# Kernel tuning notes

Hardware: AMD Instinct MI355X
Metric: run time of the kernel (lower is better)

## Reference

```python
import jax, jax.numpy as jnp
import numpy as np

EPS = 1e-5

def _layernorm(x, g, b):
    m = jnp.mean(x, axis=-1, keepdims=True)
    v = jnp.mean((x - m) ** 2, axis=-1, keepdims=True)
    return (x - m) * jax.lax.rsqrt(v + EPS) * g + b

def setup_inputs() -> dict:
    key = jax.random.key(0)
    ks = jax.random.split(key, 6)
    B, N, D, H, F = 4, 4096, 256, 256, 1024
    s = lambda d: 1.0 / np.sqrt(d)
    return {
        "x": jax.random.normal(ks[0], (B, N, D), jnp.float32),
        "ln1_g": jnp.ones((D,), jnp.float32),
        "ln1_b": jnp.zeros((D,), jnp.float32),
        "wq": jax.random.normal(ks[1], (D, H), jnp.float32) * s(D),
        "bq": jnp.zeros((H,), jnp.float32),
        "wk": jax.random.normal(ks[2], (D, H), jnp.float32) * s(D),
        "bk": jnp.zeros((H,), jnp.float32),
        "wv": jax.random.normal(ks[3], (D, D), jnp.float32) * s(D),
        "bv": jnp.zeros((D,), jnp.float32),
        "ln2_g": jnp.ones((D,), jnp.float32),
        "ln2_b": jnp.zeros((D,), jnp.float32),
        "w1": jax.random.normal(ks[4], (D, F), jnp.float32) * s(D),
        "b1": jnp.zeros((F,), jnp.float32),
        "w2": jax.random.normal(ks[5], (F, D), jnp.float32) * s(F),
        "b2": jnp.zeros((D,), jnp.float32),
    }

def reference(x, ln1_g, ln1_b, wq, bq, wk, bk, wv, bv, ln2_g, ln2_b, w1, b1, w2, b2):
    hdim = wq.shape[1]
    x = _layernorm(x, ln1_g, ln1_b)                      # [B,N,D]
    q = x @ wq + bq                                      # [B,N,H]
    k = x @ wk + bk                                      # [B,N,H]
    v = x @ wv + bv                                      # [B,N,D]
    att = jnp.einsum('bnh,bmh->bnm', q, k) / jnp.sqrt(jnp.float32(hdim))
    att = jax.nn.softmax(att, axis=-1)                   # [B,N,N]
    x = jnp.einsum('bnm,bmd->bnd', att, v) + x           # residual around attention
    h = _layernorm(x, ln2_g, ln2_b)
    h = jax.nn.relu(h @ w1 + b1) @ w2 + b2
    return h + x
```

## Files before the change

### kernel.cpp

```cpp
#include <hip/hip_runtime.h>
#include <stdint.h>

typedef unsigned short u16;
typedef __attribute__((ext_vector_type(8))) short short8;
typedef __attribute__((ext_vector_type(4))) float f32x4;
typedef __attribute__((ext_vector_type(16))) float f32x16;

__device__ __forceinline__ u16 f2b(float f){
  union { float f; unsigned u; } x; x.f = f;
  unsigned r = x.u + 0x7FFFu + ((x.u >> 16) & 1u);
  return (u16)(r >> 16);
}
__device__ __forceinline__ float b2f(u16 u){
  return __uint_as_float(((unsigned)u) << 16);
}

__device__ __forceinline__ unsigned cvtpk_bf16(float lo, float hi){
  unsigned r;
  asm("v_cvt_pk_bf16_f32 %0, %1, %2" : "=v"(r) : "v"(lo), "v"(hi));
  return r;
}

__device__ __forceinline__ void gload_lds16(const void* g, void* l){
  __builtin_amdgcn_global_load_lds(
      (const __attribute__((address_space(1))) unsigned int*)g,
      (__attribute__((address_space(3))) unsigned int*)l, 16, 0, 0);
}

__global__ void __launch_bounds__(256) transpose_all(const float* __restrict__ wq,
                                                     const float* __restrict__ wk,
                                                     const float* __restrict__ wv,
                                                     const float* __restrict__ w1,
                                                     const float* __restrict__ w2,
                                                     u16* __restrict__ wqkvT,
                                                     u16* __restrict__ w1T,
                                                     u16* __restrict__ w2T){
  __shared__ float sm[32][33];
  int id = blockIdx.x;
  const float* in; u16* out; int K, N, kx, ny;
  if (id < 192){
    int j = id >> 6, r = id & 63;
    in = (j==0) ? wq : (j==1) ? wk : wv;
    out = wqkvT + (size_t)j*65536; K = 256; N = 256; kx = r>>3; ny = r&7;
  } else if (id < 448){
    int r = id - 192; in = w1; out = w1T; K = 256; N = 1024; kx = r&7; ny = r>>3;
  } else {
    int r = id - 448; in = w2; out = w2T; K = 1024; N = 256; kx = r>>3; ny = r&7;
  }
  int k0 = kx*32, n0 = ny*32;
  int t = threadIdx.x; int tr = t>>5, tc = t&31;
  #pragma unroll
  for (int p=0;p<4;p++) sm[p*8+tr][tc] = in[(size_t)(k0+p*8+tr)*N + n0+tc];
  __syncthreads();
  #pragma unroll
  for (int p=0;p<4;p++) out[(size_t)(n0+p*8+tr)*K + k0+tc] = f2b(sm[tc][p*8+tr]);
}

__global__ void __launch_bounds__(256) ln_kernel(const float* __restrict__ in,
                                                 const float* __restrict__ g,
                                                 const float* __restrict__ bb,
                                                 float* __restrict__ outF,
                                                 u16* __restrict__ outB){
  int row = blockIdx.x, t = threadIdx.x;
  size_t base = (size_t)row*256;
  float v = in[base + t];
  float s = v;
  #pragma unroll
  for (int m=1;m<64;m<<=1) s += __shfl_xor(s, m);
  __shared__ float red[4];
  int w = t>>6;
  if ((t&63)==0) red[w] = s;
  __syncthreads();
  float mean = (red[0]+red[1]+red[2]+red[3]) * (1.0f/256.0f);
  float d = v - mean;
  float s2 = d*d;
  #pragma unroll
  for (int m=1;m<64;m<<=1) s2 += __shfl_xor(s2, m);
  __syncthreads();
  if ((t&63)==0) red[w] = s2;
  __syncthreads();
  float var = (red[0]+red[1]+red[2]+red[3]) * (1.0f/256.0f);
  float y = d * rsqrtf(var + 1e-5f) * g[t] + bb[t];
  if (outF) outF[base+t] = y;
  outB[base+t] = f2b(y);
}

template<int MODE>
__global__ void __launch_bounds__(256, 2) gemm_bt(const u16* __restrict__ A,
                                                  const u16* __restrict__ BT,
                                                  const float* __restrict__ bias,
                                                  const float* __restrict__ bias2,
                                                  const float* __restrict__ bias3,
                                                  const u16* __restrict__ res,
                                                  float* __restrict__ outF,
                                                  u16* __restrict__ outB,
                                                  u16* __restrict__ outB2,
                                                  u16* __restrict__ outB3,
                                                  int M, int N, int K){
  __shared__ u16 As[128*64];
  __shared__ u16 Bs[128*64];
  int tid = threadIdx.x;
  int m0 = blockIdx.x*128, n0 = blockIdx.y*128;
  int wave = tid>>6, lane = tid&63, lr = lane&15, lg = lane>>4;
  int wm = (wave>>1)*64, wn = (wave&1)*64;

  f32x4 acc[4][4];
  #pragma unroll
  for (int i=0;i<4;i++)
    #pragma unroll
    for (int j=0;j<4;j++) acc[i][j] = (f32x4){0.f,0.f,0.f,0.f};

  int nk = K >> 6;
  for (int kt=0; kt<nk; ++kt){
    __syncthreads();
    #pragma unroll
    for (int i=0;i<4;i++){
      int de = i*256 + tid; int row = de>>3; int ch = de&7; int sc = ch ^ (row&7);
      gload_lds16(A + (size_t)(m0+row)*K + kt*64 + sc*8, (char*)As + de*16);
    }
    #pragma unroll
    for (int i=0;i<4;i++){
      int de = i*256 + tid; int row = de>>3; int ch = de&7; int sc = ch ^ (row&7);
      gload_lds16(BT + (size_t)(n0+row)*K + kt*64 + sc*8, (char*)Bs + de*16);
    }
    asm volatile("s_waitcnt vmcnt(0)" ::: "memory");
    __syncthreads();
    #pragma unroll
    for (int kk=0;kk<2;kk++){
      short8 af[4], bf[4];
      #pragma unroll
      for (int mi=0;mi<4;mi++){
        int row = wm + mi*16 + lr;
        int c = (kk*4 + lg) ^ (row&7);
        af[mi] = *(const short8*)&As[row*64 + c*8];
      }
      #pragma unroll
      for (int ni=0;ni<4;ni++){
        int row = wn + ni*16 + lr;
        int c = (kk*4 + lg) ^ (row&7);
        bf[ni] = *(const short8*)&Bs[row*64 + c*8];
      }
      #pragma unroll
      for (int mi=0;mi<4;mi++)
        #pragma unroll
        for (int ni=0;ni<4;ni++)
          acc[mi][ni] = __builtin_amdgcn_mfma_f32_16x16x32_bf16(af[mi], bf[ni], acc[mi][ni], 0,0,0);
    }
  }
  #pragma unroll
  for (int mi=0;mi<4;mi++)
    #pragma unroll
    for (int ni=0;ni<4;ni++)
      #pragma unroll
      for (int r=0;r<4;r++){
        int row = m0 + wm + mi*16 + lg*4 + r;
        int col = n0 + wn + ni*16 + lr;
        if (MODE==3){
          int seg = n0 >> 8;
          int c2 = col & 255;
          float bb = (seg==0) ? bias[c2] : (seg==1) ? bias2[c2] : bias3[c2];
          float vout = acc[mi][ni][r] + bb;
          if (seg==0)      outB [(size_t)row*256 + c2] = f2b(vout);
          else if (seg==1) outB2[(size_t)row*256 + c2] = f2b(vout);
          else {
            size_t gaddr = ((size_t)(row>>12)<<20)
                         + ((((size_t)((row&4095)>>3)<<8) + (size_t)c2)<<3) + (row&7);
            outB3[gaddr] = f2b(vout);
          }
        } else {
          float vout = acc[mi][ni][r] + bias[col];
          if (MODE==1) vout = fmaxf(vout, 0.f);
          if (MODE==2) outF[(size_t)row*N + col] = vout + b2f(res[(size_t)row*N + col]);
          else         outB[(size_t)row*N + col] = f2b(vout);
        }
      }
}

__device__ __forceinline__ void stage_tiles(const u16* __restrict__ Kb,
                                            const u16* __restrict__ Vt,
                                            int b, int kv0,
                                            char* Kdst, char* Vdst, int tid){
  #pragma unroll
  for (int i=0;i<4;i++){
    int de = i*256 + tid; int kv = de>>5; int c = de&31; int sc = c ^ (kv&7);
    gload_lds16(Kb + (((size_t)(b*4096 + kv0 + kv))<<8) + sc*8, Kdst + (size_t)de*16);
  }
  #pragma unroll
  for (int i=0;i<4;i++){
    int de = i*256 + tid; int kvc = de>>8; int d = de&255;
    gload_lds16(Vt + ((((size_t)b*512 + (kv0>>3) + kvc)<<8) + (size_t)d)*8,
                Vdst + (size_t)de*16);
  }
}

__global__ void __launch_bounds__(256, 2) flash_attn32(const u16* __restrict__ Qb,
                                                       const u16* __restrict__ Kb,
                                                       const u16* __restrict__ Vt,
                                                       u16* __restrict__ Opart,
                                                       float* __restrict__ MLpart){
  __shared__ __align__(16) char smem[74752];
  const int NC = 4096;
  int tid = threadIdx.x, wave = tid>>6, lane = tid&63;
  int lq = lane & 31, hi = lane >> 5;
  int b = blockIdx.y, s = blockIdx.z;
  int qb0 = blockIdx.x*128 + wave*32;
  int kvbeg = s*1024;
  const int NT = 32;
  u16* PsW = (u16*)(smem + 65536) + wave*32*36;

  short8 qf[16];
  {
    const u16* qbase = Qb + (((size_t)b*NC + qb0 + lq)<<8) + hi*8;
    #pragma unroll
    for (int ks=0; ks<16; ks++) qf[ks] = *(const short8*)(qbase + ks*16);
  }

  f32x16 o[8];
  #pragma unroll
  for (int i=0;i<8;i++)
    o[i] = (f32x16){0.f,0.f,0.f,0.f,0.f,0.f,0.f,0.f,0.f,0.f,0.f,0.f,0.f,0.f,0.f,0.f};
  float mrun = -__builtin_inff(), ell = 0.f;

  stage_tiles(Kb, Vt, b, kvbeg, smem, smem + 16384, tid);
  asm volatile("s_waitcnt vmcnt(0)" ::: "memory");
  __syncthreads();

  for (int t=0; t<NT; t++){
    char* Kc = smem + ((t&1) ? 32768 : 0);
    char* Vc = Kc + 16384;
    char* Kn = smem + ((t&1) ? 0 : 32768);
    char* Vn = Kn + 16384;
    int kv0 = kvbeg + t*32;
    if (t+1 < NT) stage_tiles(Kb, Vt, b, kv0+32, Kn, Vn, tid);

    f32x16 sacc = (f32x16){0.f,0.f,0.f,0.f,0.f,0.f,0.f,0.f,0.f,0.f,0.f,0.f,0.f,0.f,0.f,0.f};
    __builtin_amdgcn_s_setprio(1);
    #pragma unroll
    for (int ks=0; ks<16; ks++){
      int c = ks*2 + hi;
      short8 kf = *(const short8*)(Kc + lq*512 + ((c ^ (lq&7))<<4));
      sacc = __builtin_amdgcn_mfma_f32_32x32x16_bf16(kf, qf[ks], sacc, 0,0,0);
    }
    __builtin_amdgcn_s_setprio(0);

    float tmax = sacc[0];
    #pragma unroll
    for (int r=1;r<16;r++) tmax = fmaxf(tmax, sacc[r]);
    tmax *= 0.0625f;
    tmax = fmaxf(tmax, __shfl_xor(tmax, 32));
    if (!__all(tmax <= mrun + 8.f)){
      float mn = fmaxf(mrun, tmax);
      float sc = __expf(mrun - mn);
      mrun = mn; ell *= sc;
      #pragma unroll
      for (int r=0;r<16;r++){
        float scr = __shfl(sc, (r&3)+8*(r>>2)+4*hi);
        #pragma unroll
        for (int dt=0; dt<8; dt++) o[dt][r] *= scr;
      }
    }

    float rs = 0.f;
    #pragma unroll
    for (int h=0; h<2; h++){
      float p[8];
      #pragma unroll
      for (int r=0;r<8;r++){ p[r] = __expf(sacc[h*8+r]*0.0625f - mrun); rs += p[r]; }
      uint2 w0, w1;
      w0.x = cvtpk_bf16(p[0], p[1]);  w0.y = cvtpk_bf16(p[2], p[3]);
      w1.x = cvtpk_bf16(p[4], p[5]);  w1.y = cvtpk_bf16(p[6], p[7]);
      *(uint2*)(PsW + lq*36 + h*16 + hi*4)     = w0;
      *(uint2*)(PsW + lq*36 + h*16 + 8 + hi*4) = w1;
    }
    rs += __shfl_xor(rs, 32);
    ell += rs;
    asm volatile("s_waitcnt lgkmcnt(0)" ::: "memory");
    __builtin_amdgcn_sched_barrier(0);
    union { uint2 u2[2]; short8 s8; } pc0, pc1;
    pc0.u2[0] = *(const uint2*)(PsW + lq*36 + hi*8);
    pc0.u2[1] = *(const uint2*)(PsW + lq*36 + hi*8 + 4);
    pc1.u2[0] = *(const uint2*)(PsW + lq*36 + 16 + hi*8);
    pc1.u2[1] = *(const uint2*)(PsW + lq*36 + 16 + hi*8 + 4);
    short8 pa0 = pc0.s8, pa1 = pc1.s8;

    __builtin_amdgcn_s_setprio(1);
    #pragma unroll
    for (int dt=0; dt<8; dt++){
      short8 vf0 = *(const short8*)(Vc + (((hi  )*256 + dt*32 + lq)<<4));
      short8 vf1 = *(const short8*)(Vc + (((2+hi)*256 + dt*32 + lq)<<4));
      o[dt] = __builtin_amdgcn_mfma_f32_32x32x16_bf16(pa0, vf0, o[dt], 0,0,0);
      o[dt] = __builtin_amdgcn_mfma_f32_32x32x16_bf16(pa1, vf1, o[dt], 0,0,0);
    }
    __builtin_amdgcn_s_setprio(0);

    asm volatile("s_waitcnt vmcnt(0)" ::: "memory");
    __syncthreads();
  }

  size_t rowb = (size_t)s*16384 + (size_t)b*NC + qb0;
  #pragma unroll
  for (int dt=0; dt<8; dt++)
    #pragma unroll
    for (int r=0;r<16;r++){
      int q = (r&3) + 8*(r>>2) + 4*hi;
      Opart[(rowb + q)*256 + dt*32 + lq] = f2b(o[dt][r]);
    }
  if (lane < 32){
    MLpart[(rowb + lane)*2]     = mrun;
    MLpart[(rowb + lane)*2 + 1] = ell;
  }
}

__global__ void __launch_bounds__(256) merge4_ln(const u16* __restrict__ Opart,
                                                 const float* __restrict__ MLpart,
                                                 const float* __restrict__ xln,
                                                 const float* __restrict__ g2,
                                                 const float* __restrict__ be2,
                                                 u16* __restrict__ x2b,
                                                 u16* __restrict__ h2){
  int row = blockIdx.x; int t = threadIdx.x;
  const size_t RS = 16384ull*256;
  float m[4], l[4];
  #pragma unroll
  for (int s=0;s<4;s++){
    m[s] = MLpart[((size_t)s*16384 + row)*2];
    l[s] = MLpart[((size_t)s*16384 + row)*2 + 1];
  }
  float M = fmaxf(fmaxf(m[0],m[1]), fmaxf(m[2],m[3]));
  float e[4]; float den = 0.f;
  #pragma unroll
  for (int s=0;s<4;s++){ e[s] = __expf(m[s]-M); den += l[s]*e[s]; }
  float inv = 1.0f/den;
  size_t idx = (size_t)row*256 + t;
  float v = 0.f;
  #pragma unroll
  for (int s=0;s<4;s++) v += b2f(Opart[(size_t)s*RS + idx]) * e[s];
  v = v*inv + xln[idx];
  x2b[idx] = f2b(v);
  float s1 = v;
  #pragma unroll
  for (int mk=1;mk<64;mk<<=1) s1 += __shfl_xor(s1, mk);
  __shared__ float red[4];
  int w = t>>6;
  if ((t&63)==0) red[w] = s1;
  __syncthreads();
  float mean = (red[0]+red[1]+red[2]+red[3]) * (1.0f/256.0f);
  float d = v - mean;
  float s2 = d*d;
  #pragma unroll
  for (int mk=1;mk<64;mk<<=1) s2 += __shfl_xor(s2, mk);
  __syncthreads();
  if ((t&63)==0) red[w] = s2;
  __syncthreads();
  float var = (red[0]+red[1]+red[2]+red[3]) * (1.0f/256.0f);
  h2[idx] = f2b(d * rsqrtf(var + 1e-5f) * g2[t] + be2[t]);
}

extern "C" void kernel_launch(void* const* d_in, const int* in_sizes, int n_in,
                              void* d_out, int out_size, void* d_ws, size_t ws_size,
                              hipStream_t stream){
  const float* x   = (const float*)d_in[0];
  const float* g1  = (const float*)d_in[1];
  const float* be1 = (const float*)d_in[2];
  const float* wq  = (const float*)d_in[3];
  const float* bq  = (const float*)d_in[4];
  const float* wk  = (const float*)d_in[5];
  const float* bk  = (const float*)d_in[6];
  const float* wv  = (const float*)d_in[7];
  const float* bv  = (const float*)d_in[8];
  const float* g2  = (const float*)d_in[9];
  const float* be2 = (const float*)d_in[10];
  const float* w1  = (const float*)d_in[11];
  const float* bm1 = (const float*)d_in[12];
  const float* w2  = (const float*)d_in[13];
  const float* bm2 = (const float*)d_in[14];
  float* out = (float*)d_out;

  const size_t RS = 16384ull*256;
  char* p = (char*)d_ws;
  float* xln = (float*)p;  p += RS*4;
  u16*  Op   = (u16*)p;    p += 4*RS*2;
  float* ML  = (float*)p;  p += 4*16384ull*2*4;
  u16* xb  = (u16*)p; p += RS*2;
  u16* qb  = (u16*)p; p += RS*2;
  u16* kb  = (u16*)p; p += RS*2;
  u16* vT  = (u16*)p; p += RS*2;
  u16* x2b = (u16*)p; p += RS*2;
  u16* wqkvT = (u16*)p; p += 3*65536ull*2;
  u16* w1T = (u16*)p; p += 262144ull*2;
  u16* w2T = (u16*)p; p += 262144ull*2;
  u16*   h1 = Op;
  u16*   h2 = qb;

  transpose_all<<<704, 256, 0, stream>>>(wq, wk, wv, w1, w2, wqkvT, w1T, w2T);

  ln_kernel<<<16384,256,0,stream>>>(x, g1, be1, xln, xb);

  gemm_bt<3><<<dim3(128,6),256,0,stream>>>(xb, wqkvT, bq, bk, bv, nullptr, nullptr,
                                           qb, kb, vT, 16384,768,256);

  flash_attn32<<<dim3(32,4,4),256,0,stream>>>(qb, kb, vT, Op, ML);
  merge4_ln<<<16384,256,0,stream>>>(Op, ML, xln, g2, be2, x2b, h2);

  gemm_bt<1><<<dim3(128,8),256,0,stream>>>(h2, w1T, bm1, nullptr, nullptr, nullptr, nullptr,
                                           h1, nullptr, nullptr, 16384,1024,256);
  gemm_bt<2><<<dim3(128,2),256,0,stream>>>(h1, w2T, bm2, nullptr, nullptr, x2b, out,
                                           nullptr, nullptr, nullptr, 16384,256,1024);
}
```

Before: 167.1 us.

## Keep softmax P in registers by permuting the V layout to match accumulators

Removes the per-wave LDS round trip that converted the S accumulator layout into the MFMA A-operand layout for P. Instead, the P values are packed straight from registers, and the projection kernel writes the transposed V with a permuted row order so the kv index matches the accumulator ordering. This drops the LDS writes, the lgkmcnt wait and the LDS reads in each tile, and shrinks shared memory, which may help occupancy. The risk is correctness: the permutation has to agree exactly with the MFMA output register mapping.

```diff
diff --git a/kernel.cpp b/kernel.cpp
--- a/kernel.cpp
+++ b/kernel.cpp
@@ -163,8 +163,12 @@
           if (seg==0)      outB [(size_t)row*256 + c2] = f2b(vout);
           else if (seg==1) outB2[(size_t)row*256 + c2] = f2b(vout);
           else {
-            size_t gaddr = ((size_t)(row>>12)<<20)
-                         + ((((size_t)((row&4095)>>3)<<8) + (size_t)c2)<<3) + (row&7);
+            int n = row & 4095;
+            int u = n & 31;
+            int g = ((u>>2)&1) | (((u>>4)&1)<<1);
+            int j = (u&3) | (((u>>3)&1)<<2);
+            size_t gran = (size_t)((n>>5)<<2) + g;
+            size_t gaddr = ((size_t)(row>>12)<<20) + (((gran<<8) + (size_t)c2)<<3) + j;
             outB3[gaddr] = f2b(vout);
           }
         } else {
@@ -198,7 +202,7 @@
                                                        const u16* __restrict__ Vt,
                                                        u16* __restrict__ Opart,
                                                        float* __restrict__ MLpart){
-  __shared__ __align__(16) char smem[74752];
+  __shared__ __align__(16) char smem[65536];
   const int NC = 4096;
   int tid = threadIdx.x, wave = tid>>6, lane = tid&63;
   int lq = lane & 31, hi = lane >> 5;
@@ -206,7 +210,6 @@
   int qb0 = blockIdx.x*128 + wave*32;
   int kvbeg = s*1024;
   const int NT = 32;
-  u16* PsW = (u16*)(smem + 65536) + wave*32*36;
 
   short8 qf[16];
   {
@@ -261,27 +264,18 @@
     }
 
     float rs = 0.f;
-    #pragma unroll
-    for (int h=0; h<2; h++){
-      float p[8];
-      #pragma unroll
-      for (int r=0;r<8;r++){ p[r] = __expf(sacc[h*8+r]*0.0625f - mrun); rs += p[r]; }
-      uint2 w0, w1;
-      w0.x = cvtpk_bf16(p[0], p[1]);  w0.y = cvtpk_bf16(p[2], p[3]);
-      w1.x = cvtpk_bf16(p[4], p[5]);  w1.y = cvtpk_bf16(p[6], p[7]);
-      *(uint2*)(PsW + lq*36 + h*16 + hi*4)     = w0;
-      *(uint2*)(PsW + lq*36 + h*16 + 8 + hi*4) = w1;
-    }
+    float pv[16];
+    #pragma unroll
+    for (int r=0;r<16;r++){ pv[r] = __expf(sacc[r]*0.0625f - mrun); rs += pv[r]; }
     rs += __shfl_xor(rs, 32);
     ell += rs;
-    asm volatile("s_waitcnt lgkmcnt(0)" ::: "memory");
-    __builtin_amdgcn_sched_barrier(0);
-    union { uint2 u2[2]; short8 s8; } pc0, pc1;
-    pc0.u2[0] = *(const uint2*)(PsW + lq*36 + hi*8);
-    pc0.u2[1] = *(const uint2*)(PsW + lq*36 + hi*8 + 4);
-    pc1.u2[0] = *(const uint2*)(PsW + lq*36 + 16 + hi*8);
-    pc1.u2[1] = *(const uint2*)(PsW + lq*36 + 16 + hi*8 + 4);
-    short8 pa0 = pc0.s8, pa1 = pc1.s8;
+    union { unsigned w[4]; short8 s; } c0, c1;
+    #pragma unroll
+    for (int r=0;r<4;r++){
+      c0.w[r] = cvtpk_bf16(pv[2*r],   pv[2*r+1]);
+      c1.w[r] = cvtpk_bf16(pv[8+2*r], pv[8+2*r+1]);
+    }
+    short8 pa0 = c0.s, pa1 = c1.s;
 
     __builtin_amdgcn_s_setprio(1);
     #pragma unroll
```

New measurement: 164.0 us. About the same (-1.9%).
